# Kernel optimization log

Measured on AMD Instinct MI355X. Metric: run time of the kernel, lower is better.

The kernel has to match this reference:

```python
import jax, jax.numpy as jnp
import numpy as np

S, N, C_M, C_Z, C, H = 256, 384, 64, 128, 32, 8


def _layer_norm(x, w, b, eps=1e-5):
    mu = x.mean(axis=-1, keepdims=True)
    var = x.var(axis=-1, keepdims=True)
    return (x - mu) / jnp.sqrt(var + eps) * w + b


def setup_inputs() -> dict:
    key = jax.random.key(0)
    ks = jax.random.split(key, 8)
    m = jax.random.normal(ks[0], (S, N, C_M), dtype=jnp.float32)
    z = jax.random.normal(ks[1], (N, N, C_Z), dtype=jnp.float32)
    single_mask = jax.random.bernoulli(ks[2], 0.9, (N,))
    scale = 0.02
    return {
        "m": m,
        "z": z,
        "single_mask": single_mask,
        "ln_m_w": jnp.ones((C_M,), jnp.float32),
        "ln_m_b": jnp.zeros((C_M,), jnp.float32),
        "ln_z_w": jnp.ones((C_Z,), jnp.float32),
        "ln_z_b": jnp.zeros((C_Z,), jnp.float32),
        "w_v": jax.random.normal(ks[3], (C_M, H * C), jnp.float32) * scale,
        "w_b": jax.random.normal(ks[4], (C_Z, H), jnp.float32) * scale,
        "w_g": jax.random.normal(ks[5], (C_M, H * C), jnp.float32) * scale,
        "w_out": jax.random.normal(ks[6], (H * C, C_M), jnp.float32) * scale,
    }


def reference(m, z, single_mask, ln_m_w, ln_m_b, ln_z_w, ln_z_b, w_v, w_b, w_g, w_out):
    # m: [s, i, c_m], z: [i, j, c_z], single_mask: [j] bool
    m_ln = _layer_norm(m, ln_m_w, ln_m_b)
    v = (m_ln @ w_v).reshape(S, N, H, C)          # [s, j, h, c]
    b = _layer_norm(z, ln_z_w, ln_z_b) @ w_b      # [i, j, h]
    g = jax.nn.sigmoid(m_ln @ w_g)                # [s, i, h*c]
    # mask broadcast over j axis: [..., None, :, None]
    b = b + jnp.where(single_mask[None, :, None], 0.0, -1e9)
    w = jax.nn.softmax(b, axis=-2)                # softmax over j
    o = jnp.einsum('ijh,sjhc->sihc', w, v)        # [s, i, h, c]
    o = g * o.reshape(S, N, H * C)
    return o @ w_out                               # [s, i, c_m]
```

## Files before the change

kernel.cpp:

```cpp
#include <hip/hip_runtime.h>
#include <math.h>


#define SS 256
#define NN 384
#define CM 64
#define CZ 128
#define HH 8
#define HC 256
#define NV 25165824

typedef __attribute__((ext_vector_type(8))) short short8v;
typedef __attribute__((ext_vector_type(8))) unsigned short ushort8v;
typedef __attribute__((ext_vector_type(4))) unsigned short ushort4v;
typedef __attribute__((ext_vector_type(4))) float f32x4;

static __device__ __forceinline__ float bf2f(unsigned short u) {
    union { unsigned int i; float f; } x; x.i = ((unsigned int)u) << 16; return x.f;
}
static __device__ __forceinline__ unsigned short f2bf(float f) {
    union { float f; unsigned int i; } x; x.f = f;
    unsigned int r = x.i + 0x7FFFu + ((x.i >> 16) & 1u);
    return (unsigned short)(r >> 16);
}
static __device__ __forceinline__ void gload_lds16(const void* g, void* l) {
    __builtin_amdgcn_global_load_lds((const __attribute__((address_space(1))) void*)g,
                                     (__attribute__((address_space(3))) void*)l, 16, 0, 0);
}

__global__ __launch_bounds__(256) void k_prep(
    const unsigned int* __restrict__ mu, const float* __restrict__ lnzw,
    const float* __restrict__ lnzb, const float* __restrict__ w_b,
    const float* __restrict__ w_v, const float* __restrict__ w_g,
    float* __restrict__ mterm, unsigned short* __restrict__ w2bf,
    float* __restrict__ consts, unsigned short* __restrict__ BTg)
{
    const int b = blockIdx.x, tid = threadIdx.x;
    if (b == 0) {
        __shared__ int byteLayout;
        if (tid == 0) byteLayout = 0;
        __syncthreads();
        if (tid < 96) {
            unsigned int u = mu[tid];
            if (u != 0u && u != 1u && u != 0x3F800000u) atomicOr(&byteLayout, 1);
        }
        __syncthreads();
        for (int j = tid; j < 384; j += 256) {
            int val;
            if (byteLayout) val = ((const unsigned char*)mu)[j];
            else            val = (mu[j] != 0u);
            mterm[j] = val ? 0.0f : -1e9f;
        }
    } else if (b == 1) {
        __shared__ float pA[128][8], pB[128][8];
        const int c = tid & 127;
        if (tid < 128) {
            float lw = lnzw[c], lb = lnzb[c];
            float4 wb0 = *(const float4*)&w_b[c * 8];
            float4 wb1 = *(const float4*)&w_b[c * 8 + 4];
            float wv[8] = {wb0.x, wb0.y, wb0.z, wb0.w, wb1.x, wb1.y, wb1.z, wb1.w};
            #pragma unroll
            for (int h = 0; h < 8; h++) {
                w2bf[h * CZ + c]       = f2bf(lw * wv[h]);
                w2bf[(8 + h) * CZ + c] = 0;
                pA[c][h] = lw * wv[h];
                pB[c][h] = lb * wv[h];
            }
        }
        __syncthreads();
        if (tid < 8) {
            float A = 0.f, B = 0.f;
            for (int q = 0; q < 128; q++) { A += pA[q][tid]; B += pB[q][tid]; }
            consts[tid] = A; consts[16 + tid] = B;
            consts[8 + tid] = 0.f; consts[24 + tid] = 0.f;
        }
    } else {
        const int col = (b - 2) * 4 + (tid >> 6);
        const int k   = tid & 63;
        float w = (col < 256) ? w_v[k * 256 + col] : w_g[k * 256 + (col - 256)];
        BTg[col * 64 + (k ^ ((col & 7) << 3))] = f2bf(w);
    }
}

__global__ __launch_bounds__(512) void k1b_vg(
    const unsigned short* __restrict__ BTg, const float* __restrict__ m,
    const float* __restrict__ lnw, const float* __restrict__ lnb,
    unsigned short* __restrict__ vT, unsigned short* __restrict__ gout)
{
    __shared__ unsigned short Wl[32768];
    __shared__ unsigned short Al[4096];
    const int tid = threadIdx.x, wid = tid >> 6, lane = tid & 63;
    const int rl = lane & 15, kc = lane >> 4;
    const int fam = wid >> 2, wq = wid & 3;
    const int rowBase = blockIdx.x * 64;
    const int s = rowBase / NN, j0 = rowBase - s * NN;

    const float lw = lnw[lane], lb = lnb[lane];
    float mx[8];
    #pragma unroll
    for (int rr = 0; rr < 8; rr++)
        mx[rr] = m[(size_t)(rowBase + wid * 8 + rr) * CM + lane];
    __builtin_amdgcn_sched_barrier(0);

    #pragma unroll
    for (int it = 0; it < 8; it++) {
        int eoff = wid * 4096 + it * 512;
        gload_lds16(BTg + eoff + lane * 8, (void*)((char*)Wl + eoff * 2));
    }
    __builtin_amdgcn_sched_barrier(0);

    #pragma unroll
    for (int rr = 0; rr < 8; rr++) {
        int row = wid * 8 + rr;
        float x = mx[rr];
        float s1 = x, s2 = x * x;
        #pragma unroll
        for (int off = 32; off; off >>= 1) {
            s1 += __shfl_xor(s1, off);
            s2 += __shfl_xor(s2, off);
        }
        float mu  = s1 * (1.0f / CM);
        float var = s2 * (1.0f / CM) - mu * mu;
        float y = (x - mu) * rsqrtf(var + 1e-5f) * lw + lb;
        Al[row * 64 + (lane ^ ((row & 7) << 3))] = f2bf(y);
    }

    asm volatile("s_waitcnt lgkmcnt(0)" ::: "memory");
    __builtin_amdgcn_s_barrier();
    __builtin_amdgcn_sched_barrier(0);
    asm volatile("s_waitcnt vmcnt(0)" ::: "memory");
    __builtin_amdgcn_sched_barrier(0);

    short8v al[2][4];
    #pragma unroll
    for (int ks = 0; ks < 2; ks++)
        #pragma unroll
        for (int q = 0; q < 4; q++) {
            int row = q * 16 + rl;
            al[ks][q] = *(const short8v*)&Al[(row * 64 + ks * 32 + kc * 8) ^ ((row & 7) << 3)];
        }

    unsigned short* WP = Wl + wid * 4096;
    unsigned short* VS = WP;

    f32x4 acc[4][4] = {};
    if (fam == 0) {
        #pragma unroll
        for (int ks = 0; ks < 2; ks++) {
            short8v wf[4];
            #pragma unroll
            for (int q = 0; q < 4; q++) {
                int cl = q * 16 + rl;
                wf[q] = *(const short8v*)&WP[(cl * 64 + ks * 32 + kc * 8) ^ ((cl & 7) << 3)];
            }
            #pragma unroll
            for (int mi = 0; mi < 4; mi++)
                #pragma unroll
                for (int nf = 0; nf < 4; nf++)
                    acc[mi][nf] = __builtin_amdgcn_mfma_f32_16x16x32_bf16(al[ks][mi], wf[nf], acc[mi][nf], 0, 0, 0);
        }
        #pragma unroll
        for (int mi = 0; mi < 4; mi++) {
            const int jb = mi * 16 + kc * 4;
            #pragma unroll
            for (int nf = 0; nf < 4; nf++) {
                int hcl = nf * 16 + rl;
                ushort4v o4;
                #pragma unroll
                for (int r = 0; r < 4; r++) o4[r] = f2bf(acc[mi][nf][r]);
                *(ushort4v*)&VS[(hcl * 64 + jb) ^ ((hcl & 7) << 3)] = o4;
            }
        }
        #pragma unroll
        for (int p = 0; p < 8; p++) {
            int hcl = p * 8 + (lane >> 3);
            int j8  = (lane & 7) * 8;
            ushort8v val = *(const ushort8v*)&VS[(hcl * 64 + j8) ^ ((hcl & 7) << 3)];
            int hc = wq * 64 + hcl;
            size_t vrow = (size_t)((hc >> 5) * 8192 + s * 32 + (hc & 31));
            *(ushort8v*)&vT[vrow * NN + j0 + j8] = val;
        }
    } else {
        #pragma unroll
        for (int ks = 0; ks < 2; ks++) {
            short8v wf[4];
            #pragma unroll
            for (int q = 0; q < 4; q++) {
                int cl = q * 16 + rl;
                wf[q] = *(const short8v*)&WP[(cl * 64 + ks * 32 + kc * 8) ^ ((cl & 7) << 3)];
            }
            #pragma unroll
            for (int mi = 0; mi < 4; mi++)
                #pragma unroll
                for (int nf = 0; nf < 4; nf++)
                    acc[mi][nf] = __builtin_amdgcn_mfma_f32_16x16x32_bf16(wf[mi], al[ks][nf], acc[mi][nf], 0, 0, 0);
        }
        #pragma unroll
        for (int mi = 0; mi < 4; mi++) {
            const int hcb = mi * 16 + kc * 4;
            #pragma unroll
            for (int nf = 0; nf < 4; nf++) {
                int rowl = nf * 16 + rl;
                ushort4v o4;
                #pragma unroll
                for (int r = 0; r < 4; r++)
                    o4[r] = f2bf(1.0f / (1.0f + __expf(-acc[mi][nf][r])));
                *(ushort4v*)&VS[(rowl * 64 + hcb) ^ ((rowl & 7) << 3)] = o4;
            }
        }
        #pragma unroll
        for (int p = 0; p < 8; p++) {
            int rowl = p * 8 + (lane >> 3);
            int hc8  = (lane & 7) * 8;
            ushort8v val = *(const ushort8v*)&VS[(rowl * 64 + hc8) ^ ((rowl & 7) << 3)];
            *(ushort8v*)&gout[(size_t)(rowBase + rowl) * HC + wq * 64 + hc8] = val;
        }
    }
}

__global__ __launch_bounds__(256) void k2_mfma(
    const float* __restrict__ z, const unsigned short* __restrict__ w2bf,
    const float* __restrict__ consts, const float* __restrict__ mterm,
    unsigned short* __restrict__ wbl)
{
    __shared__ float st[4][16][2];
    const int tid = threadIdx.x, wid = tid >> 6, lane = tid & 63;
    const int rl = lane & 15, kc = lane >> 4;
    const int rowBase = blockIdx.x * 64 + wid * 16;
    const int i = rowBase / NN, j0 = rowBase - i * NN;
    const float* zr = z + (size_t)(rowBase + rl) * CZ + kc * 8;

    float s1 = 0.f, s2 = 0.f;
    short8v af[4];
    #pragma unroll
    for (int ks = 0; ks < 4; ks++) {
        float4 z0 = *(const float4*)(zr + ks * 32);
        float4 z1 = *(const float4*)(zr + ks * 32 + 4);
        float zz[8] = {z0.x, z0.y, z0.z, z0.w, z1.x, z1.y, z1.z, z1.w};
        short8v a;
        #pragma unroll
        for (int q = 0; q < 8; q++) {
            s1 += zz[q];
            s2 += zz[q] * zz[q];
            a[q] = (short)f2bf(zz[q]);
        }
        af[ks] = a;
    }
    s1 += __shfl_xor(s1, 16); s2 += __shfl_xor(s2, 16);
    s1 += __shfl_xor(s1, 32); s2 += __shfl_xor(s2, 32);
    if (kc == 0) { st[wid][rl][0] = s1; st[wid][rl][1] = s2; }

    f32x4 acc = {};
    #pragma unroll
    for (int ks = 0; ks < 4; ks++) {
        short8v b = *(const short8v*)&w2bf[rl * CZ + ks * 32 + kc * 8];
        acc = __builtin_amdgcn_mfma_f32_16x16x32_bf16(af[ks], b, acc, 0, 0, 0);
    }
    __syncthreads();

    const float Ah = consts[rl], Bh = consts[16 + rl];
    unsigned short pv[4];
    #pragma unroll
    for (int reg = 0; reg < 4; reg++) {
        int r = 4 * kc + reg;
        float S1 = st[wid][r][0], S2 = st[wid][r][1];
        float mu   = S1 * (1.0f / CZ);
        float var  = S2 * (1.0f / CZ) - mu * mu;
        float rstd = rsqrtf(var + 1e-5f);
        float b = rstd * acc[reg] - rstd * mu * Ah + Bh + mterm[j0 + r];
        pv[reg] = f2bf(b);
    }
    if (rl < 8) {
        ushort4v o4 = {pv[0], pv[1], pv[2], pv[3]};
        *(ushort4v*)&wbl[((size_t)rl * NN + i) * NN + j0 + 4 * kc] = o4;
    }
}

__global__ __launch_bounds__(256) void k3_softmax(unsigned short* __restrict__ wbl)
{
    const int tid = threadIdx.x, wave = tid >> 6, lane = tid & 63;
    const int row = blockIdx.x * 4 + wave;
    unsigned short* p = wbl + (size_t)row * NN;
    float x[6];
    float mx = -1e30f;
    #pragma unroll
    for (int e = 0; e < 6; e++) { x[e] = bf2f(p[lane + e * 64]); mx = fmaxf(mx, x[e]); }
    #pragma unroll
    for (int off = 32; off; off >>= 1) mx = fmaxf(mx, __shfl_xor(mx, off));
    float sum = 0.f;
    #pragma unroll
    for (int e = 0; e < 6; e++) { x[e] = expf(x[e] - mx); sum += x[e]; }
    #pragma unroll
    for (int off = 32; off; off >>= 1) sum += __shfl_xor(sum, off);
    float inv = 1.0f / sum;
    #pragma unroll
    for (int e = 0; e < 6; e++) p[lane + e * 64] = f2bf(x[e] * inv);
}

__global__ __launch_bounds__(256) void k4_mfma(
    const unsigned short* __restrict__ wbf, const unsigned short* __restrict__ vT,
    unsigned short* __restrict__ ob)
{
    __shared__ unsigned short Al[128 * 32];
    __shared__ unsigned short Bl[128 * 32];
    const int tid  = threadIdx.x;
    const int wid  = tid >> 6, lane = tid & 63;
    const int wm   = wid >> 1, wn = wid & 1;
    const int h    = blockIdx.z;
    const int i0   = blockIdx.y * 128;
    const int n0   = blockIdx.x * 128;
    const unsigned short* Ag = wbf + (size_t)h * NN * NN;
    const unsigned short* Bg = vT  + (size_t)h * 8192 * NN;

    f32x4 acc[4][4] = {};

    const int lrow = lane >> 2, lchunk = lane & 3;
    for (int k0 = 0; k0 < NN; k0 += 32) {
        #pragma unroll
        for (int q = 0; q < 2; q++) {
            int issue = wid * 2 + q;
            int r = issue * 16 + lrow;
            gload_lds16(Ag + (size_t)(i0 + r) * NN + k0 + lchunk * 8,
                        (void*)((char*)Al + issue * 1024));
            gload_lds16(Bg + (size_t)(n0 + r) * NN + k0 + lchunk * 8,
                        (void*)((char*)Bl + issue * 1024));
        }
        __syncthreads();

        short8v a[4], b[4];
        #pragma unroll
        for (int mi = 0; mi < 4; mi++)
            a[mi] = *(const short8v*)&Al[(wm * 64 + mi * 16 + (lane & 15)) * 32 + (lane >> 4) * 8];
        #pragma unroll
        for (int ni = 0; ni < 4; ni++)
            b[ni] = *(const short8v*)&Bl[(wn * 64 + ni * 16 + (lane & 15)) * 32 + (lane >> 4) * 8];
        #pragma unroll
        for (int mi = 0; mi < 4; mi++)
            #pragma unroll
            for (int ni = 0; ni < 4; ni++)
                acc[mi][ni] = __builtin_amdgcn_mfma_f32_16x16x32_bf16(b[ni], a[mi], acc[mi][ni], 0, 0, 0);
        __syncthreads();
    }

    #pragma unroll
    for (int mi = 0; mi < 4; mi++) {
        const int i = i0 + wm * 64 + mi * 16 + (lane & 15);
        #pragma unroll
        for (int ni = 0; ni < 4; ni++) {
            const int sc0 = n0 + wn * 64 + ni * 16 + ((lane >> 4) << 2);
            const int s = sc0 >> 5, c0 = sc0 & 31;
            ushort4v o4;
            #pragma unroll
            for (int r = 0; r < 4; r++) o4[r] = f2bf(acc[mi][ni][r]);
            *(ushort4v*)&ob[((size_t)s * NN + i) * HC + (h << 5) + c0] = o4;
        }
    }
}

__global__ __launch_bounds__(256) void k5_mfma(
    const unsigned short* __restrict__ ob, const unsigned short* __restrict__ g,
    const float* __restrict__ w_out, float* __restrict__ out)
{
    __shared__ unsigned short WT[64 * 256];
    const int tid = threadIdx.x, wid = tid >> 6, lane = tid & 63;
    #pragma unroll
    for (int e = 0; e < 16; e++) {
        int fidx = (tid + e * 256) * 4;
        float4 w4 = *(const float4*)&w_out[fidx];
        int k = fidx >> 6, c0 = fidx & 63;
        float wv[4] = {w4.x, w4.y, w4.z, w4.w};
        #pragma unroll
        for (int q = 0; q < 4; q++) {
            int c = c0 + q;
            WT[(((c << 8) + k)) ^ ((c & 7) << 3)] = f2bf(wv[q]);
        }
    }
    __syncthreads();

    const size_t rowbase = (size_t)blockIdx.x * 64 + wid * 16;
    const int arow = lane & 15, achunk = lane >> 4;
    const unsigned short* op = ob + (rowbase + arow) * HC + achunk * 8;
    const unsigned short* gp = g  + (rowbase + arow) * HC + achunk * 8;

    f32x4 acc[4] = {};
    #pragma unroll
    for (int ks = 0; ks < 8; ks++) {
        ushort8v o8 = *(const ushort8v*)(op + ks * 32);
        ushort8v g8 = *(const ushort8v*)(gp + ks * 32);
        short8v a;
        #pragma unroll
        for (int q = 0; q < 8; q++)
            a[q] = (short)f2bf(bf2f(o8[q]) * bf2f(g8[q]));
        #pragma unroll
        for (int nf = 0; nf < 4; nf++) {
            const int c = nf * 16 + arow;
            short8v b = *(const short8v*)&WT[(((c << 8) + ks * 32 + achunk * 8)) ^ ((c & 7) << 3)];
            acc[nf] = __builtin_amdgcn_mfma_f32_16x16x32_bf16(a, b, acc[nf], 0, 0, 0);
        }
    }
    #pragma unroll
    for (int nf = 0; nf < 4; nf++)
        #pragma unroll
        for (int r = 0; r < 4; r++)
            out[(rowbase + achunk * 4 + r) * CM + nf * 16 + arow] = acc[nf][r];
}

extern "C" void kernel_launch(void* const* d_in, const int* in_sizes, int n_in,
                              void* d_out, int out_size, void* d_ws, size_t ws_size,
                              hipStream_t stream)
{
    const float* m      = (const float*)d_in[0];
    const float* z      = (const float*)d_in[1];
    const unsigned int* mask_raw = (const unsigned int*)d_in[2];
    const float* ln_m_w = (const float*)d_in[3];
    const float* ln_m_b = (const float*)d_in[4];
    const float* ln_z_w = (const float*)d_in[5];
    const float* ln_z_b = (const float*)d_in[6];
    const float* w_v    = (const float*)d_in[7];
    const float* w_b    = (const float*)d_in[8];
    const float* w_g    = (const float*)d_in[9];
    const float* w_out  = (const float*)d_in[10];
    float* out = (float*)d_out;

    float* mterm = (float*)d_ws;
    unsigned short* wbl = (unsigned short*)(mterm + 384);
    unsigned short* vT  = wbl + 1179648;
    unsigned short* g   = vT + NV;
    unsigned short* ob  = g + NV;
    unsigned short* BTg = ob + NV;
    unsigned short* w2bf = BTg + 32768;
    float* consts = (float*)(w2bf + 2048);

    k_prep<<<130, 256, 0, stream>>>(mask_raw, ln_z_w, ln_z_b, w_b, w_v, w_g,
                                    mterm, w2bf, consts, BTg);
    k1b_vg<<<1536, 512, 0, stream>>>(BTg, m, ln_m_w, ln_m_b, vT, g);
    k2_mfma<<<2304, 256, 0, stream>>>(z, w2bf, consts, mterm, wbl);
    k3_softmax<<<768, 256, 0, stream>>>(wbl);
    k4_mfma<<<dim3(64, 3, 8), 256, 0, stream>>>(wbl, vT, ob);
    k5_mfma<<<1536, 256, 0, stream>>>(ob, g, w_out, out);
}
```

Baseline: 127.3 us.

## Fuse pair-bias LayerNorm projection with softmax over j in one kernel

```diff
diff --git a/kernel.cpp b/kernel.cpp
--- a/kernel.cpp
+++ b/kernel.cpp
@@ -218,73 +218,76 @@
     }
 }
 
-__global__ __launch_bounds__(256) void k2_mfma(
+__global__ __launch_bounds__(512) void k23_lnz_softmax(
     const float* __restrict__ z, const unsigned short* __restrict__ w2bf,
     const float* __restrict__ consts, const float* __restrict__ mterm,
     unsigned short* __restrict__ wbl)
 {
-    __shared__ float st[4][16][2];
+    __shared__ unsigned short Llog[384 * 10];
     const int tid = threadIdx.x, wid = tid >> 6, lane = tid & 63;
     const int rl = lane & 15, kc = lane >> 4;
-    const int rowBase = blockIdx.x * 64 + wid * 16;
-    const int i = rowBase / NN, j0 = rowBase - i * NN;
-    const float* zr = z + (size_t)(rowBase + rl) * CZ + kc * 8;
-
-    float s1 = 0.f, s2 = 0.f;
-    short8v af[4];
-    #pragma unroll
-    for (int ks = 0; ks < 4; ks++) {
-        float4 z0 = *(const float4*)(zr + ks * 32);
-        float4 z1 = *(const float4*)(zr + ks * 32 + 4);
-        float zz[8] = {z0.x, z0.y, z0.z, z0.w, z1.x, z1.y, z1.z, z1.w};
-        short8v a;
-        #pragma unroll
-        for (int q = 0; q < 8; q++) {
-            s1 += zz[q];
-            s2 += zz[q] * zz[q];
-            a[q] = (short)f2bf(zz[q]);
-        }
-        af[ks] = a;
-    }
-    s1 += __shfl_xor(s1, 16); s2 += __shfl_xor(s2, 16);
-    s1 += __shfl_xor(s1, 32); s2 += __shfl_xor(s2, 32);
-    if (kc == 0) { st[wid][rl][0] = s1; st[wid][rl][1] = s2; }
-
-    f32x4 acc = {};
-    #pragma unroll
-    for (int ks = 0; ks < 4; ks++) {
-        short8v b = *(const short8v*)&w2bf[rl * CZ + ks * 32 + kc * 8];
-        acc = __builtin_amdgcn_mfma_f32_16x16x32_bf16(af[ks], b, acc, 0, 0, 0);
+    const int i = blockIdx.x;
+
+    short8v bf[4];
+    #pragma unroll
+    for (int ks = 0; ks < 4; ks++)
+        bf[ks] = *(const short8v*)&w2bf[rl * CZ + ks * 32 + kc * 8];
+    const float Ah = consts[rl], Bh = consts[16 + rl];
+
+    #pragma unroll
+    for (int ch = 0; ch < 3; ch++) {
+        const int jb = wid * 48 + ch * 16;
+        const float* zr = z + ((size_t)i * NN + jb + rl) * CZ + kc * 8;
+
+        float s1 = 0.f, s2 = 0.f;
+        short8v af[4];
+        #pragma unroll
+        for (int ks = 0; ks < 4; ks++) {
+            float4 z0 = *(const float4*)(zr + ks * 32);
+            float4 z1 = *(const float4*)(zr + ks * 32 + 4);
+            float zz[8] = {z0.x, z0.y, z0.z, z0.w, z1.x, z1.y, z1.z, z1.w};
+            short8v a;
+            #pragma unroll
+            for (int q = 0; q < 8; q++) {
+                s1 += zz[q];
+                s2 += zz[q] * zz[q];
+                a[q] = (short)f2bf(zz[q]);
+            }
+            af[ks] = a;
+        }
+        s1 += __shfl_xor(s1, 16); s2 += __shfl_xor(s2, 16);
+        s1 += __shfl_xor(s1, 32); s2 += __shfl_xor(s2, 32);
+
+        f32x4 acc = {};
+        #pragma unroll
+        for (int ks = 0; ks < 4; ks++)
+            acc = __builtin_amdgcn_mfma_f32_16x16x32_bf16(af[ks], bf[ks], acc, 0, 0, 0);
+
+        unsigned short pv[4];
+        #pragma unroll
+        for (int reg = 0; reg < 4; reg++) {
+            int r = 4 * kc + reg;
+            float S1 = __shfl(s1, r);
+            float S2 = __shfl(s2, r);
+            float mu   = S1 * (1.0f / CZ);
+            float var  = S2 * (1.0f / CZ) - mu * mu;
+            float rstd = rsqrtf(var + 1e-5f);
+            float b = rstd * acc[reg] - rstd * mu * Ah + Bh + mterm[jb + r];
+            pv[reg] = f2bf(b);
+        }
+        if (rl < 8) {
+            #pragma unroll
+            for (int reg = 0; reg < 4; reg++)
+                Llog[(jb + 4 * kc + reg) * 10 + rl] = pv[reg];
+        }
     }
     __syncthreads();
 
-    const float Ah = consts[rl], Bh = consts[16 + rl];
-    unsigned short pv[4];
-    #pragma unroll
-    for (int reg = 0; reg < 4; reg++) {
-        int r = 4 * kc + reg;
-        float S1 = st[wid][r][0], S2 = st[wid][r][1];
-        float mu   = S1 * (1.0f / CZ);
-        float var  = S2 * (1.0f / CZ) - mu * mu;
-        float rstd = rsqrtf(var + 1e-5f);
-        float b = rstd * acc[reg] - rstd * mu * Ah + Bh + mterm[j0 + r];
-        pv[reg] = f2bf(b);
-    }
-    if (rl < 8) {
-        ushort4v o4 = {pv[0], pv[1], pv[2], pv[3]};
-        *(ushort4v*)&wbl[((size_t)rl * NN + i) * NN + j0 + 4 * kc] = o4;
-    }
-}
-
-__global__ __launch_bounds__(256) void k3_softmax(unsigned short* __restrict__ wbl)
-{
-    const int tid = threadIdx.x, wave = tid >> 6, lane = tid & 63;
-    const int row = blockIdx.x * 4 + wave;
-    unsigned short* p = wbl + (size_t)row * NN;
+    unsigned short* p = wbl + ((size_t)wid * NN + i) * NN;
     float x[6];
     float mx = -1e30f;
     #pragma unroll
-    for (int e = 0; e < 6; e++) { x[e] = bf2f(p[lane + e * 64]); mx = fmaxf(mx, x[e]); }
+    for (int e = 0; e < 6; e++) { x[e] = bf2f(Llog[(lane + e * 64) * 10 + wid]); mx = fmaxf(mx, x[e]); }
     #pragma unroll
     for (int off = 32; off; off >>= 1) mx = fmaxf(mx, __shfl_xor(mx, off));
     float sum = 0.f;
@@ -434,8 +437,7 @@
     k_prep<<<130, 256, 0, stream>>>(mask_raw, ln_z_w, ln_z_b, w_b, w_v, w_g,
                                     mterm, w2bf, consts, BTg);
     k1b_vg<<<1536, 512, 0, stream>>>(BTg, m, ln_m_w, ln_m_b, vT, g);
-    k2_mfma<<<2304, 256, 0, stream>>>(z, w2bf, consts, mterm, wbl);
-    k3_softmax<<<768, 256, 0, stream>>>(wbl);
+    k23_lnz_softmax<<<384, 512, 0, stream>>>(z, w2bf, consts, mterm, wbl);
     k4_mfma<<<dim3(64, 3, 8), 256, 0, stream>>>(wbl, vT, ob);
     k5_mfma<<<1536, 256, 0, stream>>>(ob, g, w_out, out);
 }
```

Result: faster. 124.2 us, median of 2 (-2.4%).
